# Performance work log

Hardware: AMD Instinct MI355X
Metric: run time of the kernel (lower is better)

## Reference

```python
import jax, jax.numpy as jnp
import numpy as np

ALPHA = 0.3
N_TAGS = 50  # POS tag vocabulary size (key space of the histogram)
B, S, R = 16, 160, 40


def setup_inputs() -> dict:
    key = jax.random.key(0)
    k1, k2, k3, k4, k5, k6 = jax.random.split(key, 6)
    return {
        "a_arc": jax.random.normal(k1, (B, S, S), dtype=jnp.float32),
        "a_rel": jax.random.normal(k2, (B, S, S, R), dtype=jnp.float32),
        "s_arc": jax.random.normal(k3, (B, S, S), dtype=jnp.float32),
        "s_rel": jax.random.normal(k4, (B, S, S, R), dtype=jnp.float32),
        "adds": jax.random.randint(k5, (B, S), 0, N_TAGS, dtype=jnp.int32),
        "pos": jax.random.randint(k6, (B, S), 0, N_TAGS, dtype=jnp.int32),
        "n_tags": N_TAGS,
    }


def reference(a_arc, a_rel, s_arc, s_rel, adds, pos, n_tags):
    # Histogram accumulation: score[(t1, t2)] += a_arc[i, p1, p2]
    # where t1 = adds[i, p1], t2 = adds[i, p2].  Flatten the pair key.
    R_ = a_rel.shape[-1]
    key_add = (adds[:, :, None] * n_tags + adds[:, None, :]).reshape(-1)  # [B*S*S]
    n_seg = n_tags * n_tags
    tab_arc = jax.ops.segment_sum(a_arc.reshape(-1), key_add, num_segments=n_seg)          # [T^2]
    tab_rel = jax.ops.segment_sum(a_rel.reshape(-1, R_), key_add, num_segments=n_seg)      # [T^2, R]
    # Gather back keyed on pos-tag pairs and blend with alpha.
    key_pos = pos[:, :, None] * n_tags + pos[:, None, :]  # [B, S, S]
    s_arc_out = s_arc + tab_arc[key_pos] * ALPHA
    s_rel_out = s_rel + tab_rel[key_pos] * ALPHA
    return s_arc_out, s_rel_out
```

## Files before the change

kernel.cpp:

```cpp
#include <hip/hip_runtime.h>

#define ALPHA 0.3f
#define NT    50
#define B_    16
#define S_    160
#define RR    40
#define NROW  (B_ * S_)
#define NPAIR (B_ * S_ * S_)
#define NSEG  (NT * NT)
#define NREL  (NPAIR * RR)
#define NCOL  (NT * RR + NT)
#define CW    2052

__global__ void zero_tab(float* __restrict__ tab, int n) {
    int i = blockIdx.x * blockDim.x + threadIdx.x;
    if (i < n) tab[i] = 0.0f;
}

__global__ void build_lists(const int* __restrict__ adds,
                            int* __restrict__ colstart,
                            int* __restrict__ collist) {
    __shared__ int tags[S_];
    __shared__ int cnt[NT];
    __shared__ int start[NT + 1];
    int b   = blockIdx.x;
    int tid = threadIdx.x;
    if (tid < S_) tags[tid] = adds[b * S_ + tid];
    __syncthreads();
    if (tid < NT) {
        int c = 0;
        for (int i = 0; i < S_; i++) c += (tags[i] == tid);
        cnt[tid] = c;
    }
    __syncthreads();
    if (tid == 0) {
        int s = 0;
        for (int t = 0; t < NT; t++) { start[t] = s; s += cnt[t]; }
        start[NT] = s;
    }
    __syncthreads();
    if (tid <= NT) colstart[b * 64 + tid] = start[tid];
    if (tid < NT) {
        int slot = start[tid];
        for (int i = 0; i < S_; i++)
            if (tags[i] == tid) collist[b * S_ + slot++] = i;
    }
}

template <int TO_C>
__global__ __launch_bounds__(256) void stage1(const float* __restrict__ a_arc,
                                              const float4* __restrict__ a_rel4,
                                              const int* __restrict__ adds,
                                              const int* __restrict__ colstart,
                                              const int* __restrict__ collist,
                                              float* __restrict__ C,
                                              float* __restrict__ tab_arc,
                                              float* __restrict__ tab_rel) {
    __shared__ int s_start[NT + 1];
    __shared__ int s_list[S_];
    int row = blockIdx.x;
    int b   = row / S_;
    int tid = threadIdx.x;
    if (tid <= NT) s_start[tid] = colstart[b * 64 + tid];
    if (tid < S_)  s_list[tid]  = collist[b * S_ + tid];
    __syncthreads();

    const float4* arow  = a_rel4 + (size_t)row * (S_ * RR / 4);
    const float*  aarow = a_arc + row * S_;
    int t1 = TO_C ? 0 : adds[row];

    for (int cell = tid; cell < NT * (RR / 4); cell += 256) {
        int t2 = cell / (RR / 4);
        int q  = cell - t2 * (RR / 4);
        float4 acc = make_float4(0.f, 0.f, 0.f, 0.f);
        int e1 = s_start[t2 + 1];
        for (int e = s_start[t2]; e < e1; ++e) {
            float4 v = arow[s_list[e] * (RR / 4) + q];
            acc.x += v.x; acc.y += v.y; acc.z += v.z; acc.w += v.w;
        }
        if (TO_C) {
            ((float4*)(C + (size_t)row * CW))[cell] = acc;
        } else {
            float* dst = tab_rel + (size_t)t1 * (NT * RR) + cell * 4;
            atomicAdd(dst + 0, acc.x); atomicAdd(dst + 1, acc.y);
            atomicAdd(dst + 2, acc.z); atomicAdd(dst + 3, acc.w);
        }
    }
    if (tid < NT) {
        float acc = 0.f;
        int e1 = s_start[tid + 1];
        for (int e = s_start[tid]; e < e1; ++e) acc += aarow[s_list[e]];
        if (TO_C) C[(size_t)row * CW + NT * RR + tid] = acc;
        else      atomicAdd(tab_arc + t1 * NT + tid, acc);
    }
}

__global__ __launch_bounds__(256) void stage2(const float* __restrict__ C,
                                              const int* __restrict__ adds,
                                              const int* __restrict__ colstart,
                                              const int* __restrict__ collist,
                                              float* __restrict__ tab_arc,
                                              float* __restrict__ tab_rel) {
    int t1 = blockIdx.y;
    int c  = blockIdx.x * 256 + threadIdx.x;
    if (c >= NCOL) return;
    float acc = 0.f;
    for (int b = 0; b < B_; b++) {
        int s0 = colstart[b * 64 + t1], s1 = colstart[b * 64 + t1 + 1];
        for (int j = s0; j < s1; j++) {
            int row = b * S_ + collist[b * S_ + j];
            acc += C[(size_t)row * CW + c];
        }
    }
    if (c < NT * RR) tab_rel[t1 * (NT * RR) + c] = acc;
    else             tab_arc[t1 * NT + (c - NT * RR)] = acc;
}

template <bool KEYS>
__global__ void apply_arc(const float* __restrict__ s_arc,
                          const int* __restrict__ pos,
                          const float* __restrict__ tab_arc,
                          float* __restrict__ out,
                          int* __restrict__ keys) {
    int i = blockIdx.x * blockDim.x + threadIdx.x;
    if (i >= NPAIR) return;
    int b   = i / (S_ * S_);
    int rem = i - b * (S_ * S_);
    int p1  = rem / S_;
    int p2  = rem - p1 * S_;
    int key = pos[b * S_ + p1] * NT + pos[b * S_ + p2];
    if (KEYS) keys[i] = key;
    out[i] = s_arc[i] + ALPHA * tab_arc[key];
}

template <bool KEYS>
__global__ void apply_rel(const float4* __restrict__ s_rel,
                          const int* __restrict__ pos,
                          const int* __restrict__ keys,
                          const float4* __restrict__ tab_rel4,
                          float4* __restrict__ out) {
    int t = blockIdx.x * blockDim.x + threadIdx.x;
    if (t >= NREL / 4) return;
    int pair = t / (RR / 4);
    int q    = t - pair * (RR / 4);
    int key;
    if (KEYS) {
        key = keys[pair];
    } else {
        int b   = pair / (S_ * S_);
        int rem = pair - b * (S_ * S_);
        int p1  = rem / S_;
        int p2  = rem - p1 * S_;
        key = pos[b * S_ + p1] * NT + pos[b * S_ + p2];
    }
    float4 sv = s_rel[t];
    float4 tv = tab_rel4[key * (RR / 4) + q];
    float4 o;
    o.x = sv.x + ALPHA * tv.x;
    o.y = sv.y + ALPHA * tv.y;
    o.z = sv.z + ALPHA * tv.z;
    o.w = sv.w + ALPHA * tv.w;
    out[t] = o;
}

extern "C" void kernel_launch(void* const* d_in, const int* in_sizes, int n_in,
                              void* d_out, int out_size, void* d_ws, size_t ws_size,
                              hipStream_t stream) {
    const float*  a_arc = (const float*)d_in[0];
    const float4* a_rel = (const float4*)d_in[1];
    const float*  s_arc = (const float*)d_in[2];
    const float4* s_rel = (const float4*)d_in[3];
    const int*    adds  = (const int*)d_in[4];
    const int*    pos   = (const int*)d_in[5];

    float* tab_arc  = (float*)d_ws;
    float* tab_rel  = tab_arc + NSEG;
    int*   keys     = (int*)(tab_rel + NSEG * RR);
    int*   colstart = keys + NPAIR;
    int*   collist  = colstart + B_ * 64;
    float* C        = (float*)(collist + B_ * S_);
    C = (float*)(((uintptr_t)C + 15) & ~(uintptr_t)15);

    size_t need_lists = (size_t)(NSEG * (RR + 1)) * 4 + (size_t)NPAIR * 4
                      + (size_t)(B_ * 64 + B_ * S_) * 4 + 16;
    size_t need_full  = need_lists + (size_t)NROW * CW * 4;

    float*  out_arc = (float*)d_out;
    float4* out_rel = (float4*)(out_arc + NPAIR);

    const int BLK = 256;

    build_lists<<<B_, 192, 0, stream>>>(adds, colstart, collist);

    if (ws_size >= need_full) {
        stage1<1><<<NROW, 256, 0, stream>>>(a_arc, a_rel, adds, colstart, collist,
                                            C, nullptr, nullptr);
        dim3 g2((NCOL + 255) / 256, NT);
        stage2<<<g2, 256, 0, stream>>>(C, adds, colstart, collist, tab_arc, tab_rel);
    } else {
        int n_tab = NSEG * (RR + 1);
        zero_tab<<<(n_tab + BLK - 1) / BLK, BLK, 0, stream>>>(tab_arc, n_tab);
        stage1<0><<<NROW, 256, 0, stream>>>(a_arc, a_rel, adds, colstart, collist,
                                            nullptr, tab_arc, tab_rel);
    }

    bool have_keys = ws_size >= need_lists;
    if (have_keys) {
        apply_arc<true><<<(NPAIR + BLK - 1) / BLK, BLK, 0, stream>>>(
            s_arc, pos, tab_arc, out_arc, keys);
        apply_rel<true><<<(NREL / 4 + BLK - 1) / BLK, BLK, 0, stream>>>(
            s_rel, pos, keys, (const float4*)tab_rel, out_rel);
    } else {
        apply_arc<false><<<(NPAIR + BLK - 1) / BLK, BLK, 0, stream>>>(
            s_arc, pos, tab_arc, out_arc, nullptr);
        apply_rel<false><<<(NREL / 4 + BLK - 1) / BLK, BLK, 0, stream>>>(
            s_rel, pos, nullptr, (const float4*)tab_rel, out_rel);
    }
}
```

Measured before the change: 83.12 us.

## Group stage1 by (batch, row tag) and fuse arc/rel apply into one row kernel

Stage1 now runs one block per (batch, t1) tag group. Each block builds its tag lists in shared memory, which removes the separate build_lists launch, and reduces all rows sharing t1 directly. This shrinks the intermediate C buffer from per-row to per-(t1,b), so stage2 becomes a fixed 16-term sum with no list lookups. The two apply kernels and the keys buffer are replaced by one per-row kernel that caches pos in shared memory and writes both outputs. The cost is fewer stage1 blocks (800) with uneven work depending on tag counts, plus redundant list building in every block.

```diff
diff --git a/kernel.cpp b/kernel.cpp
--- a/kernel.cpp
+++ b/kernel.cpp
@@ -5,6 +5,7 @@
 #define B_    16
 #define S_    160
 #define RR    40
+#define Q_    (RR / 4)
 #define NROW  (B_ * S_)
 #define NPAIR (B_ * S_ * S_)
 #define NSEG  (NT * NT)
@@ -17,69 +18,59 @@
     if (i < n) tab[i] = 0.0f;
 }
 
-__global__ void build_lists(const int* __restrict__ adds,
-                            int* __restrict__ colstart,
-                            int* __restrict__ collist) {
-    __shared__ int tags[S_];
-    __shared__ int cnt[NT];
-    __shared__ int start[NT + 1];
-    int b   = blockIdx.x;
+template <int TO_C>
+__global__ __launch_bounds__(256) void stage1g(const float* __restrict__ a_arc,
+                                               const float4* __restrict__ a_rel4,
+                                               const int* __restrict__ adds,
+                                               float* __restrict__ C,
+                                               float* __restrict__ tab_arc,
+                                               float* __restrict__ tab_rel) {
+    __shared__ int s_tags[S_];
+    __shared__ int s_cnt[NT];
+    __shared__ int s_start[NT + 1];
+    __shared__ int s_list[S_];
+    int blk = blockIdx.x;
+    int b   = blk / NT;
+    int t1  = blk - b * NT;
     int tid = threadIdx.x;
-    if (tid < S_) tags[tid] = adds[b * S_ + tid];
+
+    if (tid < S_) s_tags[tid] = adds[b * S_ + tid];
     __syncthreads();
     if (tid < NT) {
         int c = 0;
-        for (int i = 0; i < S_; i++) c += (tags[i] == tid);
-        cnt[tid] = c;
+        for (int i = 0; i < S_; i++) c += (s_tags[i] == tid);
+        s_cnt[tid] = c;
     }
     __syncthreads();
     if (tid == 0) {
         int s = 0;
-        for (int t = 0; t < NT; t++) { start[t] = s; s += cnt[t]; }
-        start[NT] = s;
+        for (int t = 0; t < NT; t++) { s_start[t] = s; s += s_cnt[t]; }
+        s_start[NT] = s;
     }
     __syncthreads();
-    if (tid <= NT) colstart[b * 64 + tid] = start[tid];
     if (tid < NT) {
-        int slot = start[tid];
+        int slot = s_start[tid];
         for (int i = 0; i < S_; i++)
-            if (tags[i] == tid) collist[b * S_ + slot++] = i;
+            if (s_tags[i] == tid) s_list[slot++] = i;
     }
-}
-
-template <int TO_C>
-__global__ __launch_bounds__(256) void stage1(const float* __restrict__ a_arc,
-                                              const float4* __restrict__ a_rel4,
-                                              const int* __restrict__ adds,
-                                              const int* __restrict__ colstart,
-                                              const int* __restrict__ collist,
-                                              float* __restrict__ C,
-                                              float* __restrict__ tab_arc,
-                                              float* __restrict__ tab_rel) {
-    __shared__ int s_start[NT + 1];
-    __shared__ int s_list[S_];
-    int row = blockIdx.x;
-    int b   = row / S_;
-    int tid = threadIdx.x;
-    if (tid <= NT) s_start[tid] = colstart[b * 64 + tid];
-    if (tid < S_)  s_list[tid]  = collist[b * S_ + tid];
     __syncthreads();
 
-    const float4* arow  = a_rel4 + (size_t)row * (S_ * RR / 4);
-    const float*  aarow = a_arc + row * S_;
-    int t1 = TO_C ? 0 : adds[row];
+    int r0 = s_start[t1], r1 = s_start[t1 + 1];
 
-    for (int cell = tid; cell < NT * (RR / 4); cell += 256) {
-        int t2 = cell / (RR / 4);
-        int q  = cell - t2 * (RR / 4);
+    for (int cell = tid; cell < NT * Q_; cell += 256) {
+        int t2 = cell / Q_;
+        int q  = cell - t2 * Q_;
+        int c0 = s_start[t2], c1 = s_start[t2 + 1];
         float4 acc = make_float4(0.f, 0.f, 0.f, 0.f);
-        int e1 = s_start[t2 + 1];
-        for (int e = s_start[t2]; e < e1; ++e) {
-            float4 v = arow[s_list[e] * (RR / 4) + q];
-            acc.x += v.x; acc.y += v.y; acc.z += v.z; acc.w += v.w;
+        for (int i = r0; i < r1; ++i) {
+            const float4* arow = a_rel4 + (size_t)(b * S_ + s_list[i]) * (S_ * Q_);
+            for (int j = c0; j < c1; ++j) {
+                float4 v = arow[s_list[j] * Q_ + q];
+                acc.x += v.x; acc.y += v.y; acc.z += v.z; acc.w += v.w;
+            }
         }
         if (TO_C) {
-            ((float4*)(C + (size_t)row * CW))[cell] = acc;
+            ((float4*)(C + (size_t)(t1 * B_ + b) * CW))[cell] = acc;
         } else {
             float* dst = tab_rel + (size_t)t1 * (NT * RR) + cell * 4;
             atomicAdd(dst + 0, acc.x); atomicAdd(dst + 1, acc.y);
@@ -87,80 +78,66 @@
         }
     }
     if (tid < NT) {
+        int t2 = tid;
+        int c0 = s_start[t2], c1 = s_start[t2 + 1];
         float acc = 0.f;
-        int e1 = s_start[tid + 1];
-        for (int e = s_start[tid]; e < e1; ++e) acc += aarow[s_list[e]];
-        if (TO_C) C[(size_t)row * CW + NT * RR + tid] = acc;
-        else      atomicAdd(tab_arc + t1 * NT + tid, acc);
+        for (int i = r0; i < r1; ++i) {
+            const float* aarow = a_arc + (size_t)(b * S_ + s_list[i]) * S_;
+            for (int j = c0; j < c1; ++j) acc += aarow[s_list[j]];
+        }
+        if (TO_C) C[(size_t)(t1 * B_ + b) * CW + NT * RR + t2] = acc;
+        else      atomicAdd(&tab_arc[t1 * NT + t2], acc);
     }
 }
 
-__global__ __launch_bounds__(256) void stage2(const float* __restrict__ C,
-                                              const int* __restrict__ adds,
-                                              const int* __restrict__ colstart,
-                                              const int* __restrict__ collist,
-                                              float* __restrict__ tab_arc,
-                                              float* __restrict__ tab_rel) {
+__global__ __launch_bounds__(256) void stage2g(const float* __restrict__ C,
+                                               float* __restrict__ tab_arc,
+                                               float* __restrict__ tab_rel) {
     int t1 = blockIdx.y;
     int c  = blockIdx.x * 256 + threadIdx.x;
     if (c >= NCOL) return;
+    const float* base = C + (size_t)t1 * B_ * CW + c;
     float acc = 0.f;
-    for (int b = 0; b < B_; b++) {
-        int s0 = colstart[b * 64 + t1], s1 = colstart[b * 64 + t1 + 1];
-        for (int j = s0; j < s1; j++) {
-            int row = b * S_ + collist[b * S_ + j];
-            acc += C[(size_t)row * CW + c];
-        }
-    }
+#pragma unroll
+    for (int b = 0; b < B_; ++b) acc += base[(size_t)b * CW];
     if (c < NT * RR) tab_rel[t1 * (NT * RR) + c] = acc;
     else             tab_arc[t1 * NT + (c - NT * RR)] = acc;
 }
 
-template <bool KEYS>
-__global__ void apply_arc(const float* __restrict__ s_arc,
-                          const int* __restrict__ pos,
-                          const float* __restrict__ tab_arc,
-                          float* __restrict__ out,
-                          int* __restrict__ keys) {
-    int i = blockIdx.x * blockDim.x + threadIdx.x;
-    if (i >= NPAIR) return;
-    int b   = i / (S_ * S_);
-    int rem = i - b * (S_ * S_);
-    int p1  = rem / S_;
-    int p2  = rem - p1 * S_;
-    int key = pos[b * S_ + p1] * NT + pos[b * S_ + p2];
-    if (KEYS) keys[i] = key;
-    out[i] = s_arc[i] + ALPHA * tab_arc[key];
-}
+__global__ __launch_bounds__(256) void apply_fused(const float* __restrict__ s_arc,
+                                                   const float4* __restrict__ s_rel4,
+                                                   const int* __restrict__ pos,
+                                                   const float* __restrict__ tab_arc,
+                                                   const float4* __restrict__ tab_rel4,
+                                                   float* __restrict__ out_arc,
+                                                   float4* __restrict__ out_rel4) {
+    __shared__ int s_pos[S_];
+    int row = blockIdx.x;
+    int b   = row / S_;
+    int p1  = row - b * S_;
+    int tid = threadIdx.x;
+    if (tid < S_) s_pos[tid] = pos[b * S_ + tid];
+    __syncthreads();
+    int base = s_pos[p1] * NT;
 
-template <bool KEYS>
-__global__ void apply_rel(const float4* __restrict__ s_rel,
-                          const int* __restrict__ pos,
-                          const int* __restrict__ keys,
-                          const float4* __restrict__ tab_rel4,
-                          float4* __restrict__ out) {
-    int t = blockIdx.x * blockDim.x + threadIdx.x;
-    if (t >= NREL / 4) return;
-    int pair = t / (RR / 4);
-    int q    = t - pair * (RR / 4);
-    int key;
-    if (KEYS) {
-        key = keys[pair];
-    } else {
-        int b   = pair / (S_ * S_);
-        int rem = pair - b * (S_ * S_);
-        int p1  = rem / S_;
-        int p2  = rem - p1 * S_;
-        key = pos[b * S_ + p1] * NT + pos[b * S_ + p2];
+    const float4* srow = s_rel4  + (size_t)row * (S_ * Q_);
+    float4*       orow = out_rel4 + (size_t)row * (S_ * Q_);
+    for (int e = tid; e < S_ * Q_; e += 256) {
+        int p2 = e / Q_;
+        int q  = e - p2 * Q_;
+        float4 sv = srow[e];
+        float4 tv = tab_rel4[(base + s_pos[p2]) * Q_ + q];
+        float4 o;
+        o.x = sv.x + ALPHA * tv.x;
+        o.y = sv.y + ALPHA * tv.y;
+        o.z = sv.z + ALPHA * tv.z;
+        o.w = sv.w + ALPHA * tv.w;
+        orow[e] = o;
     }
-    float4 sv = s_rel[t];
-    float4 tv = tab_rel4[key * (RR / 4) + q];
-    float4 o;
-    o.x = sv.x + ALPHA * tv.x;
-    o.y = sv.y + ALPHA * tv.y;
-    o.z = sv.z + ALPHA * tv.z;
-    o.w = sv.w + ALPHA * tv.w;
-    out[t] = o;
+    if (tid < S_) {
+        out_arc[row * S_ + tid] = s_arc[row * S_ + tid]
+                                + ALPHA * tab_arc[base + s_pos[tid]];
+    }
 }
 
 extern "C" void kernel_launch(void* const* d_in, const int* in_sizes, int n_in,
@@ -173,47 +150,29 @@
     const int*    adds  = (const int*)d_in[4];
     const int*    pos   = (const int*)d_in[5];
 
-    float* tab_arc  = (float*)d_ws;
-    float* tab_rel  = tab_arc + NSEG;
-    int*   keys     = (int*)(tab_rel + NSEG * RR);
-    int*   colstart = keys + NPAIR;
-    int*   collist  = colstart + B_ * 64;
-    float* C        = (float*)(collist + B_ * S_);
+    float* tab_arc = (float*)d_ws;
+    float* tab_rel = tab_arc + NSEG;
+    float* C       = tab_rel + NSEG * RR;
     C = (float*)(((uintptr_t)C + 15) & ~(uintptr_t)15);
 
-    size_t need_lists = (size_t)(NSEG * (RR + 1)) * 4 + (size_t)NPAIR * 4
-                      + (size_t)(B_ * 64 + B_ * S_) * 4 + 16;
-    size_t need_full  = need_lists + (size_t)NROW * CW * 4;
+    size_t need_tab  = (size_t)(NSEG * (RR + 1)) * 4;
+    size_t need_full = need_tab + 16 + (size_t)NT * B_ * CW * 4;
 
     float*  out_arc = (float*)d_out;
     float4* out_rel = (float4*)(out_arc + NPAIR);
 
     const int BLK = 256;
 
-    build_lists<<<B_, 192, 0, stream>>>(adds, colstart, collist);
-
     if (ws_size >= need_full) {
-        stage1<1><<<NROW, 256, 0, stream>>>(a_arc, a_rel, adds, colstart, collist,
-                                            C, nullptr, nullptr);
+        stage1g<1><<<B_ * NT, 256, 0, stream>>>(a_arc, a_rel, adds, C, nullptr, nullptr);
         dim3 g2((NCOL + 255) / 256, NT);
-        stage2<<<g2, 256, 0, stream>>>(C, adds, colstart, collist, tab_arc, tab_rel);
+        stage2g<<<g2, 256, 0, stream>>>(C, tab_arc, tab_rel);
     } else {
         int n_tab = NSEG * (RR + 1);
         zero_tab<<<(n_tab + BLK - 1) / BLK, BLK, 0, stream>>>(tab_arc, n_tab);
-        stage1<0><<<NROW, 256, 0, stream>>>(a_arc, a_rel, adds, colstart, collist,
-                                            nullptr, tab_arc, tab_rel);
+        stage1g<0><<<B_ * NT, 256, 0, stream>>>(a_arc, a_rel, adds, nullptr, tab_arc, tab_rel);
     }
 
-    bool have_keys = ws_size >= need_lists;
-    if (have_keys) {
-        apply_arc<true><<<(NPAIR + BLK - 1) / BLK, BLK, 0, stream>>>(
-            s_arc, pos, tab_arc, out_arc, keys);
-        apply_rel<true><<<(NREL / 4 + BLK - 1) / BLK, BLK, 0, stream>>>(
-            s_rel, pos, keys, (const float4*)tab_rel, out_rel);
-    } else {
-        apply_arc<false><<<(NPAIR + BLK - 1) / BLK, BLK, 0, stream>>>(
-            s_arc, pos, tab_arc, out_arc, nullptr);
-        apply_rel<false><<<(NREL / 4 + BLK - 1) / BLK, BLK, 0, stream>>>(
-            s_rel, pos, nullptr, (const float4*)tab_rel, out_rel);
-    }
+    apply_fused<<<NROW, 256, 0, stream>>>(s_arc, s_rel, pos, tab_arc,
+                                          (const float4*)tab_rel, out_arc, out_rel);
 }
```

Measured after the change: 93.07 us. +12.0%, slower.
